# Optimization experiments

Hardware: AMD Instinct MI355X
Metric: run time of the kernel (lower is better)

## Reference

```python
import jax, jax.numpy as jnp
import numpy as np
import math

N, L, E_IN, MDL, H, NE = 8, 4096, 512, 512, 8, 131072
D = MDL // H


def setup_inputs() -> dict:
    key = jax.random.key(0)
    ks = jax.random.split(key, 12)
    s_in = 1.0 / math.sqrt(E_IN)
    s_md = 1.0 / math.sqrt(MDL)
    return {
        "queries": jax.random.normal(ks[0], (N, L, E_IN), jnp.float32),
        "keys": jax.random.normal(ks[1], (N, L, E_IN), jnp.float32),
        "values": jax.random.normal(ks[2], (N, L, E_IN), jnp.float32),
        "adj": jax.random.randint(ks[3], (2, NE), 0, L, jnp.int32),
        "Wq": jax.random.normal(ks[4], (MDL, E_IN), jnp.float32) * s_in,
        "bq": jnp.zeros((MDL,), jnp.float32),
        "Wk": jax.random.normal(ks[5], (MDL, E_IN), jnp.float32) * s_in,
        "bk": jnp.zeros((MDL,), jnp.float32),
        "Wv": jax.random.normal(ks[6], (MDL, E_IN), jnp.float32) * s_in,
        "bv": jnp.zeros((MDL,), jnp.float32),
        "Wfc": jax.random.normal(ks[7], (MDL, MDL), jnp.float32) * s_md,
        "bfc": jnp.zeros((MDL,), jnp.float32),
    }


def _split_head(x):
    n, l, c = x.shape
    return jnp.transpose(x.reshape(n, l, H, c // H), (0, 2, 1, 3))  # (n,h,l,d)


def reference(queries, keys, values, adj, Wq, bq, Wk, bk, Wv, bv, Wfc, bfc):
    q = _split_head(queries @ Wq.T + bq)  # (n,h,l,e)
    k = _split_head(keys @ Wk.T + bk)
    v = _split_head(values @ Wv.T + bv)
    n, h, l, e = q.shape
    temp = 1.0 / math.sqrt(e)
    row, col = adj[0], adj[1]  # query idx / key idx per edge
    # edge-wise QK dot products: (n,h,E)
    qk = temp * jnp.einsum('nhed,nhed->nhe', q[:, :, row, :], k[:, :, col, :])
    # segment softmax over edges grouped by query node (adj[0])
    qk_t = jnp.transpose(qk, (2, 0, 1))  # (E,n,h) - segment ops act on axis 0
    m = jax.ops.segment_max(qk_t, row, num_segments=l)  # (L,n,h)
    ex = jnp.exp(qk_t - m[row])
    den = jax.ops.segment_sum(ex, row, num_segments=l)
    a = ex / den[row]  # (E,n,h); dropout is identity in eval mode
    # spmm: out[i] += a[edge] * v[j] for each edge (i=row, j=col)
    vj = jnp.transpose(v[:, :, col, :], (2, 0, 1, 3))  # (E,n,h,d)
    agg = jax.ops.segment_sum(vj * a[..., None], row, num_segments=l)  # (L,n,h,d)
    out = jnp.transpose(agg, (1, 0, 2, 3)).reshape(n, l, h * e)  # (n,l,h*d)
    return out @ Wfc.T + bfc
```

## Files before the change

### kernel.cpp

```cpp
#include <hip/hip_runtime.h>
#include <cstdint>

typedef __attribute__((ext_vector_type(8))) short short8;
typedef __attribute__((ext_vector_type(4))) float f32x4;

constexpr int NB   = 8;
constexpr int L    = 4096;
constexpr int CH   = 512;
constexpr int DD   = 64;
constexpr int NE   = 131072;
constexpr int M_ROWS = NB * L;

__device__ __forceinline__ float bf2f(unsigned short u) {
    unsigned int x = ((unsigned int)u) << 16;
    float f; __builtin_memcpy(&f, &x, 4); return f;
}
__device__ __forceinline__ unsigned short f2bf(float f) {
    unsigned int x; __builtin_memcpy(&x, &f, 4);
    x += 0x7fffu + ((x >> 16) & 1u);
    return (unsigned short)(x >> 16);
}
__device__ __forceinline__ float u2f(unsigned int x) {
    float f; __builtin_memcpy(&f, &x, 4); return f;
}

__global__ __launch_bounds__(256)
void cvt8_k(const float* __restrict__ src, unsigned short* __restrict__ dst) {
    const int i = blockIdx.x * 256 + threadIdx.x;
    const float4 a = ((const float4*)src)[i * 2];
    const float4 b = ((const float4*)src)[i * 2 + 1];
    unsigned short us[8];
    us[0] = f2bf(a.x); us[1] = f2bf(a.y); us[2] = f2bf(a.z); us[3] = f2bf(a.w);
    us[4] = f2bf(b.x); us[5] = f2bf(b.y); us[6] = f2bf(b.z); us[7] = f2bf(b.w);
    ((short8*)dst)[i] = *(short8*)us;
}

__global__ __launch_bounds__(256)
void cvtw_k(const float* __restrict__ s0, const float* __restrict__ s1,
            const float* __restrict__ s2, const float* __restrict__ s3,
            unsigned short* __restrict__ dst) {
    const float* s = (blockIdx.y == 0) ? s0 : (blockIdx.y == 1) ? s1
                   : (blockIdx.y == 2) ? s2 : s3;
    unsigned short* d = dst + (size_t)blockIdx.y * (CH * CH);
    const int i = blockIdx.x * 256 + threadIdx.x;
    const float4 a = ((const float4*)s)[i * 2];
    const float4 b = ((const float4*)s)[i * 2 + 1];
    unsigned short us[8];
    us[0] = f2bf(a.x); us[1] = f2bf(a.y); us[2] = f2bf(a.z); us[3] = f2bf(a.w);
    us[4] = f2bf(b.x); us[5] = f2bf(b.y); us[6] = f2bf(b.z); us[7] = f2bf(b.w);
    ((short8*)d)[i] = *(short8*)us;
}

template <bool OUT_F32>
__global__ __launch_bounds__(256)
void gemm_bf(const unsigned short* __restrict__ A, const unsigned short* __restrict__ B,
             const float* __restrict__ bias, void* __restrict__ Cp)
{
    __shared__ unsigned short As[128 * 64];
    __shared__ unsigned short Bs[128 * 64];
    const int bid = blockIdx.x;
    const int swz = (bid & 7) * 128 + (bid >> 3);
    const int row0 = (swz >> 2) * 128;
    const int col0 = (swz & 3) * 128;
    const int t = threadIdx.x, lane = t & 63, wid = t >> 6;
    const int wm = (wid >> 1) * 64, wn = (wid & 1) * 64;
    const int fr = lane & 15, fkb = (lane >> 4) * 8;
    const int srow = lane >> 3;
    const int scol = (lane & 7) * 8;

    f32x4 acc[4][4] = {};

    for (int k0 = 0; k0 < CH; k0 += 64) {
#pragma unroll
        for (int q = 0; q < 4; q++) {
            const int r = wid * 32 + q * 8;
            __builtin_amdgcn_global_load_lds(
                (const __attribute__((address_space(1))) unsigned int*)
                    (A + (size_t)(row0 + r + srow) * CH + k0 + scol),
                (__attribute__((address_space(3))) unsigned int*)(As + r * 64),
                16, 0, 0);
        }
#pragma unroll
        for (int q = 0; q < 4; q++) {
            const int r = wid * 32 + q * 8;
            __builtin_amdgcn_global_load_lds(
                (const __attribute__((address_space(1))) unsigned int*)
                    (B + (size_t)(col0 + r + srow) * CH + k0 + scol),
                (__attribute__((address_space(3))) unsigned int*)(Bs + r * 64),
                16, 0, 0);
        }
        __syncthreads();
#pragma unroll
        for (int kk = 0; kk < 2; kk++) {
            short8 afr[4], bfr[4];
#pragma unroll
            for (int f = 0; f < 4; f++)
                afr[f] = *(const short8*)&As[(wm + f * 16 + fr) * 64 + kk * 32 + fkb];
#pragma unroll
            for (int f = 0; f < 4; f++)
                bfr[f] = *(const short8*)&Bs[(wn + f * 16 + fr) * 64 + kk * 32 + fkb];
#pragma unroll
            for (int fm = 0; fm < 4; fm++)
#pragma unroll
                for (int fn = 0; fn < 4; fn++)
                    acc[fm][fn] = __builtin_amdgcn_mfma_f32_16x16x32_bf16(
                        afr[fm], bfr[fn], acc[fm][fn], 0, 0, 0);
        }
        __syncthreads();
    }

    const int rsub = (lane >> 4) * 4;
#pragma unroll
    for (int fn = 0; fn < 4; fn++) {
        const int gc = col0 + wn + fn * 16 + fr;
        const float bv = bias[gc];
#pragma unroll
        for (int fm = 0; fm < 4; fm++) {
            const int gr = row0 + wm + fm * 16 + rsub;
#pragma unroll
            for (int j = 0; j < 4; j++) {
                float v = acc[fm][fn][j] + bv;
                if constexpr (OUT_F32)
                    ((float*)Cp)[(size_t)(gr + j) * CH + gc] = v;
                else
                    ((unsigned short*)Cp)[(size_t)(gr + j) * CH + gc] = f2bf(v);
            }
        }
    }
}

__global__ void zero_k(int* cnt, int* fill) {
    int i = blockIdx.x * blockDim.x + threadIdx.x;
    if (i < L) { cnt[i] = 0; fill[i] = 0; }
}
__global__ void count_k(const int* __restrict__ adj, int* __restrict__ cnt) {
    int e = blockIdx.x * blockDim.x + threadIdx.x;
    if (e < NE) atomicAdd(&cnt[adj[e]], 1);
}
__global__ void scan_k(const int* __restrict__ cnt, int* __restrict__ rowptr) {
    const int lane = threadIdx.x;
    const int base = lane * 64;
    int s = 0;
    for (int t2 = 0; t2 < 64; t2++) s += cnt[base + t2];
    int incl = s;
    for (int off = 1; off < 64; off <<= 1) {
        int v = __shfl_up(incl, off);
        if (lane >= off) incl += v;
    }
    int run = incl - s;
    for (int t2 = 0; t2 < 64; t2++) { rowptr[base + t2] = run; run += cnt[base + t2]; }
    if (lane == 63) rowptr[L] = run;
}
__global__ void scatter_k(const int* __restrict__ adj, const int* __restrict__ rowptr,
                          int* __restrict__ fill, int* __restrict__ ecol) {
    int e = blockIdx.x * blockDim.x + threadIdx.x;
    if (e < NE) {
        int rr = adj[e];
        int pos = rowptr[rr] + atomicAdd(&fill[rr], 1);
        ecol[pos] = adj[NE + e];
    }
}

__global__ __launch_bounds__(256)
void attn_k(const unsigned short* __restrict__ qb, const unsigned short* __restrict__ kb,
            const unsigned short* __restrict__ vb, const int* __restrict__ rowptr,
            const int* __restrict__ ecol, unsigned short* __restrict__ agg)
{
    __shared__ float part[4 * 8 * 65];
    const int bid = blockIdx.x;
    const int n   = bid & 7;
    const int rem = bid >> 3;
    const int hg  = rem >> 12;
    const int i   = rem & 4095;
    const int lane = threadIdx.x & 63;
    const int w    = threadIdx.x >> 6;
    const int h    = hg * 4 + w;
    const int g    = lane & 7;
    const int grp  = lane >> 3;
    const size_t rowbase = ((size_t)(n * L + i)) * CH + h * DD;

    constexpr float SCALE = 0.125f * 1.44269504088896f;
    float qf[8];
    {
        const short8 qu = *(const short8*)(qb + rowbase + g * 8);
        const unsigned int* qw = (const unsigned int*)&qu;
#pragma unroll
        for (int e = 0; e < 4; e++) {
            qf[2 * e]     = u2f(qw[e] << 16) * SCALE;
            qf[2 * e + 1] = u2f(qw[e] & 0xffff0000u) * SCALE;
        }
    }
    const int start = rowptr[i], end = rowptr[i + 1];
    const char* kb_nh = (const char*)(kb + (size_t)n * L * CH + h * DD);
    const char* vb_nh = (const char*)(vb + (size_t)n * L * CH + h * DD);

    float o[8] = {};
    float lsum = 0.f;

    const int nIter = (end - start + 7) >> 3;
    int idx = start + grp;
    int j = (end > start) ? ecol[idx < end ? idx : end - 1] : 0;
    for (int it = 0; it < nIter; ++it) {
        const bool valid = idx < end;
        const int off = (j << 10) + (g << 4);
        const short8 ku = *(const short8*)(kb_nh + off);
        const short8 vu = *(const short8*)(vb_nh + off);
        const int idxn = idx + 8;
        const int jn = (it + 1 < nIter) ? ecol[idxn < end ? idxn : end - 1] : 0;
        const unsigned int* kw = (const unsigned int*)&ku;
        float s = 0.f;
#pragma unroll
        for (int e = 0; e < 4; e++) {
            s = fmaf(u2f(kw[e] << 16),         qf[2 * e],     s);
            s = fmaf(u2f(kw[e] & 0xffff0000u), qf[2 * e + 1], s);
        }
        s += __shfl_xor(s, 1);
        s += __shfl_xor(s, 2);
        s += __shfl_xor(s, 4);
        s = valid ? s : -1e30f;
#if __has_builtin(__builtin_amdgcn_exp2f)
        const float pe = __builtin_amdgcn_exp2f(s);
#else
        const float pe = exp2f(s);
#endif
        const unsigned int* vw = (const unsigned int*)&vu;
#pragma unroll
        for (int e = 0; e < 4; e++) {
            o[2 * e]     = fmaf(pe, u2f(vw[e] << 16),         o[2 * e]);
            o[2 * e + 1] = fmaf(pe, u2f(vw[e] & 0xffff0000u), o[2 * e + 1]);
        }
        lsum += pe;
        idx = idxn;
        j = jn;
    }

    lsum += __shfl_xor(lsum, 8);
    lsum += __shfl_xor(lsum, 16);
    lsum += __shfl_xor(lsum, 32);

    float* p = part + w * (8 * 65);
    float* pw = p + grp * 65 + g * 8;
    *(float4*)(pw)     = *(float4*)&o[0];
    *(float4*)(pw + 4) = *(float4*)&o[4];
    __builtin_amdgcn_s_waitcnt(0);
    float osum = 0.f;
#pragma unroll
    for (int gg = 0; gg < 8; gg++)
        osum += p[gg * 65 + lane];

    const float inv = (end > start) ? 1.f / lsum : 0.f;
    agg[rowbase + lane] = f2bf(osum * inv);
}

extern "C" void kernel_launch(void* const* d_in, const int* in_sizes, int n_in,
                              void* d_out, int out_size, void* d_ws, size_t ws_size,
                              hipStream_t stream)
{
    (void)in_sizes; (void)n_in; (void)out_size; (void)ws_size;
    const float* queries = (const float*)d_in[0];
    const float* keys    = (const float*)d_in[1];
    const float* values  = (const float*)d_in[2];
    const int*   adj     = (const int*)d_in[3];
    const float* Wq  = (const float*)d_in[4];
    const float* bq  = (const float*)d_in[5];
    const float* Wk  = (const float*)d_in[6];
    const float* bk  = (const float*)d_in[7];
    const float* Wv  = (const float*)d_in[8];
    const float* bv  = (const float*)d_in[9];
    const float* Wfc = (const float*)d_in[10];
    const float* bfc = (const float*)d_in[11];

    unsigned short* qb = (unsigned short*)d_out;
    unsigned short* kb = qb + (size_t)M_ROWS * CH;
    uint8_t* w = (uint8_t*)d_ws;
    unsigned short* vb  = (unsigned short*)(w);
    unsigned short* agg = (unsigned short*)(w + 33554432);
    unsigned short* wbf = (unsigned short*)(w + 67108864);
    int* cnt    = (int*)(w + 69206016);
    int* fill   = (int*)(w + 69206016 + 16384);
    int* rowptr = (int*)(w + 69206016 + 32768);
    int* ecol   = (int*)(w + 69206016 + 65536);

    unsigned short* stg = agg;
    constexpr int WELEM = CH * CH;

    cvtw_k<<<dim3(WELEM / (256 * 8), 4), 256, 0, stream>>>(Wq, Wk, Wv, Wfc, wbf);

    dim3 gg(1024);
    cvt8_k<<<M_ROWS * CH / (256 * 8), 256, 0, stream>>>(queries, stg);
    gemm_bf<false><<<gg, 256, 0, stream>>>(stg, wbf + 0 * WELEM, bq, qb);
    cvt8_k<<<M_ROWS * CH / (256 * 8), 256, 0, stream>>>(keys, stg);
    gemm_bf<false><<<gg, 256, 0, stream>>>(stg, wbf + 1 * WELEM, bk, kb);
    cvt8_k<<<M_ROWS * CH / (256 * 8), 256, 0, stream>>>(values, stg);
    gemm_bf<false><<<gg, 256, 0, stream>>>(stg, wbf + 2 * WELEM, bv, vb);

    zero_k<<<(L + 255) / 256, 256, 0, stream>>>(cnt, fill);
    count_k<<<(NE + 255) / 256, 256, 0, stream>>>(adj, cnt);
    scan_k<<<1, 64, 0, stream>>>(cnt, rowptr);
    scatter_k<<<(NE + 255) / 256, 256, 0, stream>>>(adj, rowptr, fill, ecol);

    attn_k<<<dim3(2 * NB * L / 8 * 8 / 8 * 8), 256, 0, stream>>>(qb, kb, vb, rowptr, ecol, agg);

    gemm_bf<true><<<gg, 256, 0, stream>>>(agg, wbf + 3 * WELEM, bfc, (float*)d_out);
}
```

Baseline: 358.1 us.

## Fuse fp32-to-bf16 input conversion into projection GEMM and pack attention math

Removes the three standalone fp32->bf16 conversion kernels. The Q/K/V projection GEMMs now load fp32 activations directly, convert them in registers with v_cvt_pk_bf16_f32 and write them into a padded LDS tile, which saves a full bf16 staging write and read per input. The attention kernel rewrites its dot-product and accumulation as float2 vector operations so the compiler can emit packed FMA, drops the branch on the next-index prefetch, masks after exp2, and pads the LDS partial buffer to stride 68. The trade-off is that the A tile now goes through registers with synchronous loads instead of async global_load_lds, which may reduce load/compute overlap in the GEMM.

```diff
diff --git a/kernel.cpp b/kernel.cpp
--- a/kernel.cpp
+++ b/kernel.cpp
@@ -3,6 +3,7 @@
 
 typedef __attribute__((ext_vector_type(8))) short short8;
 typedef __attribute__((ext_vector_type(4))) float f32x4;
+typedef __attribute__((ext_vector_type(2))) float f32x2;
 
 constexpr int NB   = 8;
 constexpr int L    = 4096;
@@ -11,10 +12,6 @@
 constexpr int NE   = 131072;
 constexpr int M_ROWS = NB * L;
 
-__device__ __forceinline__ float bf2f(unsigned short u) {
-    unsigned int x = ((unsigned int)u) << 16;
-    float f; __builtin_memcpy(&f, &x, 4); return f;
-}
 __device__ __forceinline__ unsigned short f2bf(float f) {
     unsigned int x; __builtin_memcpy(&x, &f, 4);
     x += 0x7fffu + ((x >> 16) & 1u);
@@ -23,16 +20,10 @@
 __device__ __forceinline__ float u2f(unsigned int x) {
     float f; __builtin_memcpy(&f, &x, 4); return f;
 }
-
-__global__ __launch_bounds__(256)
-void cvt8_k(const float* __restrict__ src, unsigned short* __restrict__ dst) {
-    const int i = blockIdx.x * 256 + threadIdx.x;
-    const float4 a = ((const float4*)src)[i * 2];
-    const float4 b = ((const float4*)src)[i * 2 + 1];
-    unsigned short us[8];
-    us[0] = f2bf(a.x); us[1] = f2bf(a.y); us[2] = f2bf(a.z); us[3] = f2bf(a.w);
-    us[4] = f2bf(b.x); us[5] = f2bf(b.y); us[6] = f2bf(b.z); us[7] = f2bf(b.w);
-    ((short8*)dst)[i] = *(short8*)us;
+__device__ __forceinline__ unsigned int cvt_pk_bf16(float a, float b) {
+    unsigned int r;
+    asm("v_cvt_pk_bf16_f32 %0, %1, %2" : "=v"(r) : "v"(a), "v"(b));
+    return r;
 }
 
 __global__ __launch_bounds__(256)
@@ -51,12 +42,13 @@
     ((short8*)d)[i] = *(short8*)us;
 }
 
-template <bool OUT_F32>
+template <bool A_F32, bool OUT_F32>
 __global__ __launch_bounds__(256)
-void gemm_bf(const unsigned short* __restrict__ A, const unsigned short* __restrict__ B,
+void gemm_bf(const void* __restrict__ Ap, const unsigned short* __restrict__ B,
              const float* __restrict__ bias, void* __restrict__ Cp)
 {
-    __shared__ unsigned short As[128 * 64];
+    constexpr int ASTR = A_F32 ? 72 : 64;
+    __shared__ unsigned short As[128 * ASTR];
     __shared__ unsigned short Bs[128 * 64];
     const int bid = blockIdx.x;
     const int swz = (bid & 7) * 128 + (bid >> 3);
@@ -71,14 +63,29 @@
     f32x4 acc[4][4] = {};
 
     for (int k0 = 0; k0 < CH; k0 += 64) {
-#pragma unroll
-        for (int q = 0; q < 4; q++) {
-            const int r = wid * 32 + q * 8;
-            __builtin_amdgcn_global_load_lds(
-                (const __attribute__((address_space(1))) unsigned int*)
-                    (A + (size_t)(row0 + r + srow) * CH + k0 + scol),
-                (__attribute__((address_space(3))) unsigned int*)(As + r * 64),
-                16, 0, 0);
+        if constexpr (A_F32) {
+            const int r = t >> 1, ch = (t & 1) * 32;
+            const float4* ap = (const float4*)((const float*)Ap + (size_t)(row0 + r) * CH + k0 + ch);
+            unsigned int pk[16];
+#pragma unroll
+            for (int q = 0; q < 8; q++) {
+                const float4 x = ap[q];
+                pk[2 * q]     = cvt_pk_bf16(x.x, x.y);
+                pk[2 * q + 1] = cvt_pk_bf16(x.z, x.w);
+            }
+#pragma unroll
+            for (int q = 0; q < 4; q++)
+                *(uint4*)&As[r * ASTR + ch + q * 8] = *(uint4*)&pk[q * 4];
+        } else {
+#pragma unroll
+            for (int q = 0; q < 4; q++) {
+                const int r = wid * 32 + q * 8;
+                __builtin_amdgcn_global_load_lds(
+                    (const __attribute__((address_space(1))) unsigned int*)
+                        ((const unsigned short*)Ap + (size_t)(row0 + r + srow) * CH + k0 + scol),
+                    (__attribute__((address_space(3))) unsigned int*)(As + r * 64),
+                    16, 0, 0);
+            }
         }
 #pragma unroll
         for (int q = 0; q < 4; q++) {
@@ -95,7 +102,7 @@
             short8 afr[4], bfr[4];
 #pragma unroll
             for (int f = 0; f < 4; f++)
-                afr[f] = *(const short8*)&As[(wm + f * 16 + fr) * 64 + kk * 32 + fkb];
+                afr[f] = *(const short8*)&As[(wm + f * 16 + fr) * ASTR + kk * 32 + fkb];
 #pragma unroll
             for (int f = 0; f < 4; f++)
                 bfr[f] = *(const short8*)&Bs[(wn + f * 16 + fr) * 64 + kk * 32 + fkb];
@@ -166,7 +173,7 @@
             const unsigned short* __restrict__ vb, const int* __restrict__ rowptr,
             const int* __restrict__ ecol, unsigned short* __restrict__ agg)
 {
-    __shared__ float part[4 * 8 * 65];
+    __shared__ float part[4 * 8 * 68];
     const int bid = blockIdx.x;
     const int n   = bid & 7;
     const int rem = bid >> 3;
@@ -180,54 +187,56 @@
     const size_t rowbase = ((size_t)(n * L + i)) * CH + h * DD;
 
     constexpr float SCALE = 0.125f * 1.44269504088896f;
-    float qf[8];
+    f32x2 qf[4];
     {
         const short8 qu = *(const short8*)(qb + rowbase + g * 8);
         const unsigned int* qw = (const unsigned int*)&qu;
 #pragma unroll
         for (int e = 0; e < 4; e++) {
-            qf[2 * e]     = u2f(qw[e] << 16) * SCALE;
-            qf[2 * e + 1] = u2f(qw[e] & 0xffff0000u) * SCALE;
+            qf[e].x = u2f(qw[e] << 16) * SCALE;
+            qf[e].y = u2f(qw[e] & 0xffff0000u) * SCALE;
         }
     }
     const int start = rowptr[i], end = rowptr[i + 1];
     const char* kb_nh = (const char*)(kb + (size_t)n * L * CH + h * DD);
     const char* vb_nh = (const char*)(vb + (size_t)n * L * CH + h * DD);
 
-    float o[8] = {};
+    f32x2 o2[4] = {};
     float lsum = 0.f;
 
     const int nIter = (end - start + 7) >> 3;
     int idx = start + grp;
-    int j = (end > start) ? ecol[idx < end ? idx : end - 1] : 0;
+    int j = (nIter > 0) ? ecol[min(idx, end - 1)] : 0;
     for (int it = 0; it < nIter; ++it) {
         const bool valid = idx < end;
         const int off = (j << 10) + (g << 4);
         const short8 ku = *(const short8*)(kb_nh + off);
         const short8 vu = *(const short8*)(vb_nh + off);
         const int idxn = idx + 8;
-        const int jn = (it + 1 < nIter) ? ecol[idxn < end ? idxn : end - 1] : 0;
+        const int jn = ecol[min(idxn, end - 1)];
         const unsigned int* kw = (const unsigned int*)&ku;
-        float s = 0.f;
+        f32x2 s2 = {0.f, 0.f};
 #pragma unroll
         for (int e = 0; e < 4; e++) {
-            s = fmaf(u2f(kw[e] << 16),         qf[2 * e],     s);
-            s = fmaf(u2f(kw[e] & 0xffff0000u), qf[2 * e + 1], s);
-        }
+            f32x2 k2;
+            k2.x = u2f(kw[e] << 16);
+            k2.y = u2f(kw[e] & 0xffff0000u);
+            s2 += k2 * qf[e];
+        }
+        float s = s2.x + s2.y;
         s += __shfl_xor(s, 1);
         s += __shfl_xor(s, 2);
         s += __shfl_xor(s, 4);
-        s = valid ? s : -1e30f;
-#if __has_builtin(__builtin_amdgcn_exp2f)
-        const float pe = __builtin_amdgcn_exp2f(s);
-#else
-        const float pe = exp2f(s);
-#endif
+        float pe = exp2f(s);
+        pe = valid ? pe : 0.f;
         const unsigned int* vw = (const unsigned int*)&vu;
+        const f32x2 pe2 = {pe, pe};
 #pragma unroll
         for (int e = 0; e < 4; e++) {
-            o[2 * e]     = fmaf(pe, u2f(vw[e] << 16),         o[2 * e]);
-            o[2 * e + 1] = fmaf(pe, u2f(vw[e] & 0xffff0000u), o[2 * e + 1]);
+            f32x2 v2;
+            v2.x = u2f(vw[e] << 16);
+            v2.y = u2f(vw[e] & 0xffff0000u);
+            o2[e] += pe2 * v2;
         }
         lsum += pe;
         idx = idxn;
@@ -238,15 +247,15 @@
     lsum += __shfl_xor(lsum, 16);
     lsum += __shfl_xor(lsum, 32);
 
-    float* p = part + w * (8 * 65);
-    float* pw = p + grp * 65 + g * 8;
-    *(float4*)(pw)     = *(float4*)&o[0];
-    *(float4*)(pw + 4) = *(float4*)&o[4];
+    float* p = part + w * (8 * 68);
+    float* pw = p + grp * 68 + g * 8;
+    *(f32x4*)(pw)     = f32x4{o2[0].x, o2[0].y, o2[1].x, o2[1].y};
+    *(f32x4*)(pw + 4) = f32x4{o2[2].x, o2[2].y, o2[3].x, o2[3].y};
     __builtin_amdgcn_s_waitcnt(0);
     float osum = 0.f;
 #pragma unroll
     for (int gg = 0; gg < 8; gg++)
-        osum += p[gg * 65 + lane];
+        osum += p[gg * 68 + lane];
 
     const float inv = (end > start) ? 1.f / lsum : 0.f;
     agg[rowbase + lane] = f2bf(osum * inv);
@@ -281,25 +290,21 @@
     int* rowptr = (int*)(w + 69206016 + 32768);
     int* ecol   = (int*)(w + 69206016 + 65536);
 
-    unsigned short* stg = agg;
     constexpr int WELEM = CH * CH;
 
     cvtw_k<<<dim3(WELEM / (256 * 8), 4), 256, 0, stream>>>(Wq, Wk, Wv, Wfc, wbf);
 
     dim3 gg(1024);
-    cvt8_k<<<M_ROWS * CH / (256 * 8), 256, 0, stream>>>(queries, stg);
-    gemm_bf<false><<<gg, 256, 0, stream>>>(stg, wbf + 0 * WELEM, bq, qb);
-    cvt8_k<<<M_ROWS * CH / (256 * 8), 256, 0, stream>>>(keys, stg);
-    gemm_bf<false><<<gg, 256, 0, stream>>>(stg, wbf + 1 * WELEM, bk, kb);
-    cvt8_k<<<M_ROWS * CH / (256 * 8), 256, 0, stream>>>(values, stg);
-    gemm_bf<false><<<gg, 256, 0, stream>>>(stg, wbf + 2 * WELEM, bv, vb);
+    gemm_bf<true, false><<<gg, 256, 0, stream>>>(queries, wbf + 0 * WELEM, bq, qb);
+    gemm_bf<true, false><<<gg, 256, 0, stream>>>(keys,    wbf + 1 * WELEM, bk, kb);
+    gemm_bf<true, false><<<gg, 256, 0, stream>>>(values,  wbf + 2 * WELEM, bv, vb);
 
     zero_k<<<(L + 255) / 256, 256, 0, stream>>>(cnt, fill);
     count_k<<<(NE + 255) / 256, 256, 0, stream>>>(adj, cnt);
     scan_k<<<1, 64, 0, stream>>>(cnt, rowptr);
     scatter_k<<<(NE + 255) / 256, 256, 0, stream>>>(adj, rowptr, fill, ecol);
 
-    attn_k<<<dim3(2 * NB * L / 8 * 8 / 8 * 8), 256, 0, stream>>>(qb, kb, vb, rowptr, ecol, agg);
-
-    gemm_bf<true><<<gg, 256, 0, stream>>>(agg, wbf + 3 * WELEM, bfc, (float*)d_out);
-}
+    attn_k<<<dim3(2 * NB * L), 256, 0, stream>>>(qb, kb, vb, rowptr, ecol, agg);
+
+    gemm_bf<false, true><<<gg, 256, 0, stream>>>(agg, wbf + 3 * WELEM, bfc, (float*)d_out);
+}
```

Result: slower. 405.1 us (+13.1%).
